# Kernel tuning notes

Hardware: AMD Instinct MI355X
Metric: run time of the kernel (lower is better)

## Reference

```python
import jax, jax.numpy as jnp
import numpy as np

NHEAD = 16
D_MODEL = 1024
D_K = D_MODEL // NHEAD


def setup_inputs() -> dict:
    key = jax.random.key(0)
    ks = jax.random.split(key, 12)
    B, S, D = 2, 2048, D_MODEL
    scale = 1.0 / np.sqrt(D)
    inp = {
        "value": jax.random.normal(ks[0], (B, S, D), dtype=jnp.float32),
        "key": jax.random.normal(ks[1], (B, S, D), dtype=jnp.float32),
        "query": jax.random.normal(ks[2], (B, S, D), dtype=jnp.float32),
        "mask": jax.random.randint(ks[3], (B, 1, S, S), 0, 2, dtype=jnp.int32),
        "Wv": jax.random.normal(ks[4], (D, D), dtype=jnp.float32) * scale,
        "bv": jnp.zeros((D,), dtype=jnp.float32),
        "Wk": jax.random.normal(ks[5], (D, D), dtype=jnp.float32) * scale,
        "bk": jnp.zeros((D,), dtype=jnp.float32),
        "Wq": jax.random.normal(ks[6], (D, D), dtype=jnp.float32) * scale,
        "bq": jnp.zeros((D,), dtype=jnp.float32),
        "Wo": jax.random.normal(ks[7], (D, D), dtype=jnp.float32) * scale,
        "bo": jnp.zeros((D,), dtype=jnp.float32),
    }
    return inp


def reference(value, key, query, mask, Wv, bv, Wk, bk, Wq, bq, Wo, bo):
    B, S, D = value.shape
    H, Dk = NHEAD, D_K

    def proj(x, W, b):
        # nn.Linear: x @ W^T + b, then split heads -> [B, H, S, Dk]
        return (x @ W.T + b).reshape(B, S, H, Dk).transpose(0, 2, 1, 3)

    v = proj(value, Wv, bv)
    k = proj(key, Wk, bk)
    q = proj(query, Wq, bq)

    # NOTE: source code swaps K and V when calling attention():
    #   scores = Q @ V^T / sqrt(d_k);  out = softmax(scores) @ K
    scores = jnp.einsum("bhqd,bhkd->bhqk", q, v) / jnp.sqrt(jnp.float32(Dk))
    scores = jnp.where(mask == 0, jnp.float32(-1e9), scores)
    attn = jax.nn.softmax(scores, axis=-1)  # [B, H, S, S]
    attr_value = jnp.einsum("bhqk,bhkd->bhqd", attn, k)

    out = attr_value.transpose(0, 2, 1, 3).reshape(B, S, H * Dk)
    return out @ Wo.T + bo
```

## Files before the change

kernel.cpp:

```cpp
#include <hip/hip_runtime.h>

#define S_LEN 2048
#define DMODEL 1024
#define NHEADS 16
#define DKH 64

typedef __attribute__((ext_vector_type(8))) short bf16x8;
typedef __attribute__((ext_vector_type(4))) short bf16x4;
typedef __attribute__((ext_vector_type(4))) float f32x4;

#if __has_builtin(__builtin_amdgcn_exp2f)
#define EXP2F(x) __builtin_amdgcn_exp2f(x)
#define QSCALE (0.125f * 1.44269504f)
#else
#define EXP2F(x) __expf(x)
#define QSCALE 0.125f
#endif

static __device__ __forceinline__ short f2bf(float f) {
    unsigned b = __float_as_uint(f);
    b = (b + 0x7FFFu + ((b >> 16) & 1u)) >> 16;
    return (short)b;
}

static __device__ __forceinline__ unsigned pktrunc(float lo, float hi) {
#if __has_builtin(__builtin_amdgcn_perm)
    return __builtin_amdgcn_perm(__float_as_uint(hi), __float_as_uint(lo), 0x07060302u);
#else
    return (__float_as_uint(lo) >> 16) | (__float_as_uint(hi) & 0xFFFF0000u);
#endif
}

static __device__ __forceinline__ f32x4 mfma16(bf16x8 a, bf16x8 b, f32x4 c) {
    return __builtin_amdgcn_mfma_f32_16x16x32_bf16(a, b, c, 0, 0, 0);
}

static __device__ __forceinline__ bf16x8 cat44(bf16x4 a, bf16x4 b) {
    bf16x8 r;
    r[0] = a[0]; r[1] = a[1]; r[2] = a[2]; r[3] = a[3];
    r[4] = b[0]; r[5] = b[1]; r[6] = b[2]; r[7] = b[3];
    return r;
}

static __device__ __forceinline__ void glds16(const short* g, short* l) {
    __builtin_amdgcn_global_load_lds(
        (const __attribute__((address_space(1))) void*)g,
        (__attribute__((address_space(3))) void*)l, 16, 0, 0);
}

struct CvtArgs { const float* src[7]; short* dst[7]; };

__global__ __launch_bounds__(256) void prep(CvtArgs a, const int* __restrict__ mask,
                                            unsigned long long* __restrict__ mw) {
    if (blockIdx.x < 8192) {
        const size_t i8 = ((size_t)blockIdx.x * 256 + threadIdx.x) * 8;
        int seg; size_t off;
        if (i8 < ((size_t)12 << 20)) { seg = (int)(i8 >> 22); off = i8 & ((1u << 22) - 1); }
        else { size_t r = i8 - ((size_t)12 << 20); seg = 3 + (int)(r >> 20); off = r & ((1u << 20) - 1); }
        const float* s = a.src[seg] + off;
        float4 x0 = *(const float4*)s, x1 = *(const float4*)(s + 4);
        short o[8];
        o[0] = f2bf(x0.x); o[1] = f2bf(x0.y); o[2] = f2bf(x0.z); o[3] = f2bf(x0.w);
        o[4] = f2bf(x1.x); o[5] = f2bf(x1.y); o[6] = f2bf(x1.z); o[7] = f2bf(x1.w);
        *(uint4*)(a.dst[seg] + off) = *(uint4*)o;
    } else {
        const int wv = ((blockIdx.x - 8192) << 2) + (threadIdx.x >> 6);
        const int lane = threadIdx.x & 63;
        const size_t base = (size_t)wv << 4;
        #pragma unroll 4
        for (int it = 0; it < 16; ++it) {
            const size_t w = base + it;
            const int m = mask[(w << 6) + lane];
            unsigned long long bal = __ballot(m != 0);
            if (lane == 0) mw[w] = bal;
        }
    }
}

struct GemmArgs { const short* X[3]; const short* W[3]; const float* B[3];
                  void* C[3]; float scale[3]; };

template <int MODE>
__global__ __launch_bounds__(256) void gemm_bt(GemmArgs a) {
    __shared__ short Ah[128 * 32];
    __shared__ short Bh[128 * 32];
    const int z = blockIdx.z;
    const short* X = a.X[z];
    const short* W = a.W[z];
    const float* bias = a.B[z];
    const float scl = a.scale[z];

    const int t = threadIdx.x, wid = t >> 6, lane = t & 63;
    const int l15 = lane & 15, lq = lane >> 4;
    int m0, n0;
    if (MODE == 0 && z == 2) { m0 = blockIdx.y << 7; n0 = blockIdx.x << 7; }
    else                     { m0 = blockIdx.x << 7; n0 = blockIdx.y << 7; }
    const int wm = (wid >> 1) << 6, wn = (wid & 1) << 6;

    const int kb = (lane & 3) ^ ((lane >> 3) & 3);
    const int r0 = (wid << 5) + (lane >> 2);
    const short* ag0 = X + (size_t)(m0 + r0) * 1024 + (kb << 3);
    const short* ag1 = ag0 + 16 * 1024;
    const short* bg0 = W + (size_t)(n0 + r0) * 1024 + (kb << 3);
    const short* bg1 = bg0 + 16 * 1024;
    short* lA0 = Ah + (wid << 5) * 32;
    short* lA1 = lA0 + 16 * 32;
    short* lB0 = Bh + (wid << 5) * 32;
    short* lB1 = lB0 + 16 * 32;

    const int fpos = (lq ^ ((l15 >> 1) & 3)) << 3;

    f32x4 acc[4][4] = {};

    for (int k0 = 0; k0 < 1024; k0 += 32) {
        __syncthreads();
        glds16(ag0, lA0); glds16(ag1, lA1);
        glds16(bg0, lB0); glds16(bg1, lB1);
        ag0 += 32; ag1 += 32; bg0 += 32; bg1 += 32;
        __syncthreads();

        bf16x8 af[4], bfr[4];
        #pragma unroll
        for (int i = 0; i < 4; ++i)
            af[i] = *(const bf16x8*)&Ah[(wm + i * 16 + l15) * 32 + fpos];
        #pragma unroll
        for (int j = 0; j < 4; ++j)
            bfr[j] = *(const bf16x8*)&Bh[(wn + j * 16 + l15) * 32 + fpos];
        #pragma unroll
        for (int i = 0; i < 4; ++i)
            #pragma unroll
            for (int j = 0; j < 4; ++j)
                acc[i][j] = mfma16(af[i], bfr[j], acc[i][j]);
    }

    if (MODE == 0 && z == 2) {
        #pragma unroll
        for (int i = 0; i < 4; ++i) {
            #pragma unroll
            for (int r = 0; r < 4; ++r) {
                const int o = m0 + wm + i * 16 + (lq << 2) + r;
                const float bo_ = bias[o];
                const int h = o >> 6, d = o & 63;
                #pragma unroll
                for (int j = 0; j < 4; ++j) {
                    const int n = n0 + wn + j * 16 + l15;
                    const int bb = n >> 11, s = n & 2047;
                    ((short*)a.C[2])[(((size_t)((bb * 16 + h) << 6) + d) << 11) + s] =
                        f2bf(acc[i][j][r] + bo_);
                }
            }
        }
        return;
    }

    #pragma unroll
    for (int j = 0; j < 4; ++j) {
        const int n = n0 + wn + j * 16 + l15;
        const float bn = bias[n];
        #pragma unroll
        for (int i = 0; i < 4; ++i) {
            const int mbase = m0 + wm + i * 16 + (lq << 2);
            #pragma unroll
            for (int r = 0; r < 4; ++r) {
                const float val = (acc[i][j][r] + bn) * scl;
                const int m = mbase + r;
                if (MODE == 0) {
                    const int b = m >> 11, s = m & 2047, h = n >> 6, d = n & 63;
                    ((short*)a.C[z])[((((size_t)(b * 16 + h)) << 11) + s) * 64 + d] = f2bf(val);
                } else {
                    ((float*)a.C[z])[((size_t)m << 10) + n] = val;
                }
            }
        }
    }
}

__global__ __launch_bounds__(256, 4) void attn4(
    const short* __restrict__ Qh, const short* __restrict__ Vh,
    const short* __restrict__ Kt, const unsigned long long* __restrict__ MW,
    short* __restrict__ Opart, float* __restrict__ lpart)
{
    __shared__ short Vs[64 * 64];
    __shared__ short Ks[64 * 64];

    const int t = threadIdx.x, wid = t >> 6, lane = t & 63;
    const int l15 = lane & 15, lq = lane >> 4;
    const int bh = blockIdx.y, b = bh >> 4;
    const int z = blockIdx.z;
    const int ib = (blockIdx.x << 7) + (wid << 5);
    const int jbase = z << 10;

    bf16x8 qf[2][2];
    #pragma unroll
    for (int it = 0; it < 2; ++it) {
        const short* qp = Qh + ((size_t)bh * 2048 + ib + it * 16 + l15) * 64 + (lq << 3);
        qf[it][0] = *(const bf16x8*)qp;
        qf[it][1] = *(const bf16x8*)(qp + 32);
    }

    const int sr = lane >> 3, pc = lane & 7;
    const int lc = pc ^ sr;
    const int wr = wid << 4;
    const short* vsrc = Vh + (size_t)bh * 131072 + (size_t)(jbase + wr + sr) * 64 + (lc << 3);
    const short* ksrc = Kt + (size_t)bh * 131072 + (size_t)(wr + sr) * 2048 + jbase + (lc << 3);
    short* vdst = Vs + (wr << 6);
    short* kdst = Ks + (wr << 6);

    const unsigned long long* mwp0 = MW + ((size_t)b * 2048 + ib + l15) * 32 + (z << 4);
    const unsigned long long* mwp1 = mwp0 + (size_t)16 * 32;

    const int x7 = l15 & 7;
    int voff[2], koff[4];
    #pragma unroll
    for (int p = 0; p < 2; ++p) voff[p] = (((p << 2) + lq) ^ x7) << 3;
    #pragma unroll
    for (int jt = 0; jt < 4; ++jt) {
        const int c8 = (jt << 2) + lq;
        koff[jt] = (((c8 >> 1) ^ x7) << 3) + ((c8 & 1) << 2);
    }

    f32x4 O[2][4] = {};
    f32x4 lsum[2] = {};
    bf16x8 ones8;
    #pragma unroll
    for (int e = 0; e < 8; ++e) ones8[e] = (short)0x3F80;

    for (int jc = 0; jc < 16; ++jc) {
        __syncthreads();
        glds16(vsrc, vdst);
        glds16(vsrc + 512, vdst + 512);
        glds16(ksrc, kdst);
        glds16(ksrc + 8 * 2048, kdst + 512);
        vsrc += 4096; ksrc += 64;

        uint2 mword[2];
        mword[0] = *(const uint2*)(mwp0 + jc);
        mword[1] = *(const uint2*)(mwp1 + jc);
        __syncthreads();

        bf16x8 vf[4][2];
        #pragma unroll
        for (int jt = 0; jt < 4; ++jt) {
            const short* vp = &Vs[((jt << 4) + l15) << 6];
            vf[jt][0] = *(const bf16x8*)(vp + voff[0]);
            vf[jt][1] = *(const bf16x8*)(vp + voff[1]);
        }

        bf16x8 pa[2][2];
        #pragma unroll
        for (int it = 0; it < 2; ++it) {
            const unsigned wx = mword[it].x, wy = mword[it].y;
            #pragma unroll
            for (int b2 = 0; b2 < 2; ++b2) {
                uint4 uu4;
                unsigned* uw = (unsigned*)&uu4;
                #pragma unroll
                for (int h = 0; h < 2; ++h) {
                    const int jt = (b2 << 1) + h;
                    f32x4 sc = {};
                    sc = mfma16(vf[jt][0], qf[it][0], sc);
                    sc = mfma16(vf[jt][1], qf[it][1], sc);
                    const unsigned w32 = (jt < 2) ? wx : wy;
                    float p[4];
                    #pragma unroll
                    for (int r = 0; r < 4; ++r) {
                        const unsigned bit = (w32 >> (((jt & 1) << 4) + (lq << 2) + r)) & 1u;
                        const float e = EXP2F(sc[r]);
                        p[r] = bit ? e : 0.f;
                    }
                    uw[(h << 1) + 0] = pktrunc(p[0], p[1]);
                    uw[(h << 1) + 1] = pktrunc(p[2], p[3]);
                }
                pa[it][b2] = __builtin_bit_cast(bf16x8, uu4);
                lsum[it] = mfma16(pa[it][b2], ones8, lsum[it]);
            }
        }

        #pragma unroll
        for (int dt = 0; dt < 4; ++dt) {
            const short* kp = &Ks[((dt << 4) + l15) << 6];
            #pragma unroll
            for (int b2 = 0; b2 < 2; ++b2) {
                const bf16x4 k0 = *(const bf16x4*)(kp + koff[(b2 << 1) + 0]);
                const bf16x4 k1 = *(const bf16x4*)(kp + koff[(b2 << 1) + 1]);
                const bf16x8 kk = cat44(k0, k1);
                O[0][dt] = mfma16(pa[0][b2], kk, O[0][dt]);
                O[1][dt] = mfma16(pa[1][b2], kk, O[1][dt]);
            }
        }
    }

    const size_t zb = (size_t)((z << 5) + bh) * 2048;
    #pragma unroll
    for (int it = 0; it < 2; ++it) {
        const int rb = ib + (it << 4) + (lq << 2);
        if (l15 == 0) {
            #pragma unroll
            for (int r = 0; r < 4; ++r)
                lpart[zb + rb + r] = lsum[it][r];
        }
        #pragma unroll
        for (int dt = 0; dt < 4; ++dt)
            #pragma unroll
            for (int r = 0; r < 4; ++r)
                Opart[(zb + rb + r) * 64 + (dt << 4) + l15] = f2bf(O[it][dt][r]);
    }
}

__global__ __launch_bounds__(256) void combine(const short* __restrict__ Op,
                                               const float* __restrict__ lp,
                                               short* __restrict__ attr) {
    const int idx = blockIdx.x * 256 + threadIdx.x;
    const int d8 = (idx & 7) << 3;
    const int srow = (idx >> 3) & 2047;
    const int bh = idx >> 14, b = bh >> 4, h = bh & 15;
    const size_t r0 = (size_t)bh * 2048 + srow;
    const size_t r1 = r0 + (size_t)32 * 2048;
    uint4 a = *(const uint4*)(Op + r0 * 64 + d8);
    uint4 c = *(const uint4*)(Op + r1 * 64 + d8);
    const float inv = 1.f / (lp[r0] + lp[r1]);
    const unsigned* au = (const unsigned*)&a;
    const unsigned* cu = (const unsigned*)&c;
    short o[8];
    #pragma unroll
    for (int i = 0; i < 4; ++i) {
        const float a0 = __uint_as_float(au[i] << 16);
        const float a1 = __uint_as_float(au[i] & 0xFFFF0000u);
        const float c0 = __uint_as_float(cu[i] << 16);
        const float c1 = __uint_as_float(cu[i] & 0xFFFF0000u);
        o[2 * i + 0] = f2bf((a0 + c0) * inv);
        o[2 * i + 1] = f2bf((a1 + c1) * inv);
    }
    *(uint4*)&attr[((size_t)b * 2048 + srow) * 1024 + (h << 6) + d8] = *(uint4*)o;
}

extern "C" void kernel_launch(void* const* d_in, const int* in_sizes, int n_in,
                              void* d_out, int out_size, void* d_ws, size_t ws_size,
                              hipStream_t stream) {
    const float* value = (const float*)d_in[0];
    const float* key   = (const float*)d_in[1];
    const float* query = (const float*)d_in[2];
    const int*   mask  = (const int*)d_in[3];
    const float* bv = (const float*)d_in[5];
    const float* bk = (const float*)d_in[7];
    const float* bq = (const float*)d_in[9];
    const float* bo = (const float*)d_in[11];
    float* out = (float*)d_out;

    const size_t M1 = (size_t)1 << 20, M4 = (size_t)1 << 22;
    short* ws = (short*)d_ws;
    short* Xq = ws;
    short* Xk = ws + M4;
    short* Xv = ws + 2 * M4;
    short* Wc0 = ws + 3 * M4;
    short* Wc1 = Wc0 + M1;
    short* Wc2 = Wc1 + M1;
    short* Wc3 = Wc2 + M1;
    short* qh = ws + 4 * M4;
    short* kt = ws + 5 * M4;
    short* vh = ws + 6 * M4;
    unsigned long long* maskw = (unsigned long long*)(ws + 7 * M4);
    short* attr = Xq;
    short* Opart = Xk;
    float* lpart = (float*)Wc0;

    CvtArgs cv;
    cv.src[0] = query; cv.dst[0] = Xq;
    cv.src[1] = key;   cv.dst[1] = Xk;
    cv.src[2] = value; cv.dst[2] = Xv;
    cv.src[3] = (const float*)d_in[8];  cv.dst[3] = Wc0;
    cv.src[4] = (const float*)d_in[6];  cv.dst[4] = Wc1;
    cv.src[5] = (const float*)d_in[4];  cv.dst[5] = Wc2;
    cv.src[6] = (const float*)d_in[10]; cv.dst[6] = Wc3;
    prep<<<10240, 256, 0, stream>>>(cv, mask, maskw);

    GemmArgs g1;
    g1.X[0] = Xq;  g1.W[0] = Wc0; g1.B[0] = bq; g1.C[0] = qh; g1.scale[0] = QSCALE;
    g1.X[1] = Xv;  g1.W[1] = Wc2; g1.B[1] = bv; g1.C[1] = vh; g1.scale[1] = 1.f;
    g1.X[2] = Wc1; g1.W[2] = Xk;  g1.B[2] = bk; g1.C[2] = kt; g1.scale[2] = 1.f;
    gemm_bt<0><<<dim3(32, 8, 3), 256, 0, stream>>>(g1);

    attn4<<<dim3(16, 32, 2), 256, 0, stream>>>(qh, vh, kt, maskw, Opart, lpart);

    combine<<<2048, 256, 0, stream>>>(Opart, lpart, attr);

    GemmArgs g2;
    g2.X[0] = attr; g2.W[0] = Wc3; g2.B[0] = bo; g2.C[0] = out; g2.scale[0] = 1.f;
    g2.X[1] = attr; g2.W[1] = Wc3; g2.B[1] = bo; g2.C[1] = out; g2.scale[1] = 1.f;
    g2.X[2] = attr; g2.W[2] = Wc3; g2.B[2] = bo; g2.C[2] = out; g2.scale[2] = 1.f;
    gemm_bt<1><<<dim3(32, 8, 1), 256, 0, stream>>>(g2);
}
```

Measured before the change: 267.4 us.

## Double-buffer V/K tiles in LDS to overlap global loads with MFMA compute

The attention kernel now allocates two LDS buffers each for V and K. It issues the global-to-LDS loads for the next 64-key chunk, along with the next mask words, before computing on the current chunk, which drops one of the two barriers per iteration. The goal is to hide global load latency behind the QK/PV MFMA work. In exchange, LDS use per block doubles, which may reduce occupancy under launch_bounds(256,4), and the loop becomes a macro-unrolled body with a sched_barrier.

```diff
diff --git a/kernel.cpp b/kernel.cpp
--- a/kernel.cpp
+++ b/kernel.cpp
@@ -180,8 +180,10 @@
     const short* __restrict__ Kt, const unsigned long long* __restrict__ MW,
     short* __restrict__ Opart, float* __restrict__ lpart)
 {
-    __shared__ short Vs[64 * 64];
-    __shared__ short Ks[64 * 64];
+    __shared__ short Vs0[64 * 64];
+    __shared__ short Vs1[64 * 64];
+    __shared__ short Ks0[64 * 64];
+    __shared__ short Ks1[64 * 64];
 
     const int t = threadIdx.x, wid = t >> 6, lane = t & 63;
     const int l15 = lane & 15, lq = lane >> 4;
@@ -203,8 +205,7 @@
     const int wr = wid << 4;
     const short* vsrc = Vh + (size_t)bh * 131072 + (size_t)(jbase + wr + sr) * 64 + (lc << 3);
     const short* ksrc = Kt + (size_t)bh * 131072 + (size_t)(wr + sr) * 2048 + jbase + (lc << 3);
-    short* vdst = Vs + (wr << 6);
-    short* kdst = Ks + (wr << 6);
+    const int ldso = wr << 6;
 
     const unsigned long long* mwp0 = MW + ((size_t)b * 2048 + ib + l15) * 32 + (z << 4);
     const unsigned long long* mwp1 = mwp0 + (size_t)16 * 32;
@@ -225,70 +226,94 @@
     #pragma unroll
     for (int e = 0; e < 8; ++e) ones8[e] = (short)0x3F80;
 
-    for (int jc = 0; jc < 16; ++jc) {
-        __syncthreads();
-        glds16(vsrc, vdst);
-        glds16(vsrc + 512, vdst + 512);
-        glds16(ksrc, kdst);
-        glds16(ksrc + 8 * 2048, kdst + 512);
-        vsrc += 4096; ksrc += 64;
-
-        uint2 mword[2];
-        mword[0] = *(const uint2*)(mwp0 + jc);
-        mword[1] = *(const uint2*)(mwp1 + jc);
-        __syncthreads();
-
-        bf16x8 vf[4][2];
-        #pragma unroll
-        for (int jt = 0; jt < 4; ++jt) {
-            const short* vp = &Vs[((jt << 4) + l15) << 6];
-            vf[jt][0] = *(const bf16x8*)(vp + voff[0]);
-            vf[jt][1] = *(const bf16x8*)(vp + voff[1]);
-        }
-
-        bf16x8 pa[2][2];
-        #pragma unroll
-        for (int it = 0; it < 2; ++it) {
-            const unsigned wx = mword[it].x, wy = mword[it].y;
-            #pragma unroll
-            for (int b2 = 0; b2 < 2; ++b2) {
-                uint4 uu4;
-                unsigned* uw = (unsigned*)&uu4;
-                #pragma unroll
-                for (int h = 0; h < 2; ++h) {
-                    const int jt = (b2 << 1) + h;
-                    f32x4 sc = {};
-                    sc = mfma16(vf[jt][0], qf[it][0], sc);
-                    sc = mfma16(vf[jt][1], qf[it][1], sc);
-                    const unsigned w32 = (jt < 2) ? wx : wy;
-                    float p[4];
-                    #pragma unroll
-                    for (int r = 0; r < 4; ++r) {
-                        const unsigned bit = (w32 >> (((jt & 1) << 4) + (lq << 2) + r)) & 1u;
-                        const float e = EXP2F(sc[r]);
-                        p[r] = bit ? e : 0.f;
-                    }
-                    uw[(h << 1) + 0] = pktrunc(p[0], p[1]);
-                    uw[(h << 1) + 1] = pktrunc(p[2], p[3]);
-                }
-                pa[it][b2] = __builtin_bit_cast(bf16x8, uu4);
-                lsum[it] = mfma16(pa[it][b2], ones8, lsum[it]);
-            }
-        }
-
-        #pragma unroll
-        for (int dt = 0; dt < 4; ++dt) {
-            const short* kp = &Ks[((dt << 4) + l15) << 6];
-            #pragma unroll
-            for (int b2 = 0; b2 < 2; ++b2) {
-                const bf16x4 k0 = *(const bf16x4*)(kp + koff[(b2 << 1) + 0]);
-                const bf16x4 k1 = *(const bf16x4*)(kp + koff[(b2 << 1) + 1]);
-                const bf16x8 kk = cat44(k0, k1);
-                O[0][dt] = mfma16(pa[0][b2], kk, O[0][dt]);
-                O[1][dt] = mfma16(pa[1][b2], kk, O[1][dt]);
-            }
-        }
-    }
+    uint2 mc0, mc1;
+
+#define STAGE(VD, KD) do {                                       \
+        glds16(vsrc, (VD) + ldso);                               \
+        glds16(vsrc + 512, (VD) + ldso + 512);                   \
+        glds16(ksrc, (KD) + ldso);                               \
+        glds16(ksrc + 8 * 2048, (KD) + ldso + 512);              \
+        vsrc += 4096; ksrc += 64;                                \
+    } while (0)
+
+#define ABODY(VB, KB, VN, KN, JC, STG) do {                                   \
+        uint2 mn0, mn1;                                                       \
+        if (STG) {                                                            \
+            mn0 = *(const uint2*)(mwp0 + (JC) + 1);                           \
+            mn1 = *(const uint2*)(mwp1 + (JC) + 1);                           \
+            STAGE(VN, KN);                                                    \
+        }                                                                     \
+        __builtin_amdgcn_sched_barrier(0);                                    \
+                                                       \
+        bf16x8 vf[4][2];                                                      \
+        _Pragma("unroll")                                                     \
+        for (int jt = 0; jt < 4; ++jt) {                                      \
+            const short* vp = (VB) + (((jt << 4) + l15) << 6);                \
+            vf[jt][0] = *(const bf16x8*)(vp + voff[0]);                       \
+            vf[jt][1] = *(const bf16x8*)(vp + voff[1]);                       \
+        }                                                                     \
+                     \
+        bf16x8 pa[2][2];                                                      \
+        _Pragma("unroll")                                                     \
+        for (int it = 0; it < 2; ++it) {                                      \
+            const unsigned wx = (it ? mc1 : mc0).x, wy = (it ? mc1 : mc0).y;  \
+            _Pragma("unroll")                                                 \
+            for (int b2 = 0; b2 < 2; ++b2) {                                  \
+                uint4 uu4;                                                    \
+                unsigned* uw = (unsigned*)&uu4;                               \
+                _Pragma("unroll")                                             \
+                for (int h = 0; h < 2; ++h) {                                 \
+                    const int jt = (b2 << 1) + h;                             \
+                    f32x4 sc = {};                                            \
+                    sc = mfma16(vf[jt][0], qf[it][0], sc);                    \
+                    sc = mfma16(vf[jt][1], qf[it][1], sc);                    \
+                    const unsigned w32 = (jt < 2) ? wx : wy;                  \
+                    float p[4];                                               \
+                    _Pragma("unroll")                                         \
+                    for (int r = 0; r < 4; ++r) {                             \
+                        const unsigned bit =                                  \
+                            (w32 >> (((jt & 1) << 4) + (lq << 2) + r)) & 1u;  \
+                        const float e = EXP2F(sc[r]);                         \
+                        p[r] = bit ? e : 0.f;                                 \
+                    }                                                         \
+                    uw[(h << 1) + 0] = pktrunc(p[0], p[1]);                   \
+                    uw[(h << 1) + 1] = pktrunc(p[2], p[3]);                   \
+                }                                                             \
+                pa[it][b2] = __builtin_bit_cast(bf16x8, uu4);                 \
+                lsum[it] = mfma16(pa[it][b2], ones8, lsum[it]);               \
+            }                                                                 \
+        }                                                                     \
+                                                      \
+        _Pragma("unroll")                                                     \
+        for (int dt = 0; dt < 4; ++dt) {                                      \
+            const short* kp = (KB) + (((dt << 4) + l15) << 6);                \
+            _Pragma("unroll")                                                 \
+            for (int b2 = 0; b2 < 2; ++b2) {                                  \
+                const bf16x4 k0 = *(const bf16x4*)(kp + koff[(b2 << 1) + 0]); \
+                const bf16x4 k1 = *(const bf16x4*)(kp + koff[(b2 << 1) + 1]); \
+                const bf16x8 kk = cat44(k0, k1);                              \
+                O[0][dt] = mfma16(pa[0][b2], kk, O[0][dt]);                   \
+                O[1][dt] = mfma16(pa[1][b2], kk, O[1][dt]);                   \
+            }                                                                 \
+        }                                                                     \
+        __syncthreads();                                                      \
+        if (STG) { mc0 = mn0; mc1 = mn1; }                                    \
+    } while (0)
+
+    mc0 = *(const uint2*)mwp0;
+    mc1 = *(const uint2*)mwp1;
+    STAGE(Vs0, Ks0);
+    __syncthreads();
+
+    for (int jc = 0; jc < 14; jc += 2) {
+        ABODY(Vs0, Ks0, Vs1, Ks1, jc, 1);
+        ABODY(Vs1, Ks1, Vs0, Ks0, jc + 1, 1);
+    }
+    ABODY(Vs0, Ks0, Vs1, Ks1, 14, 1);
+    ABODY(Vs1, Ks1, Vs0, Ks0, 15, 0);
+
+#undef ABODY
+#undef STAGE
 
     const size_t zb = (size_t)((z << 5) + bh) * 2048;
     #pragma unroll
```

Result: slower. 340.8 us (+27.4%).
